# Kernel tuning notes

Hardware: AMD Instinct MI355X
Metric: run time of the kernel (lower is better)

The kernel has to match this reference:

```python
import jax, jax.numpy as jnp
import numpy as np

H_SIZE = 2048
NUM_K_HEADS = 16
NUM_V_HEADS = 32
DK = 128
DV = 128
KEY_DIM = NUM_K_HEADS * DK        # 2048
VALUE_DIM = NUM_V_HEADS * DV      # 4096
CONV_DIM = 2 * KEY_DIM + VALUE_DIM  # 8192
KERNEL = 4
EPS = 1e-6
B, S = 2, 2048


def setup_inputs() -> dict:
    key = jax.random.key(0)
    ks = jax.random.split(key, 8)
    w = lambda k, shape, s: jax.random.normal(k, shape, jnp.float32) * s
    return {
        "hidden_states": jax.random.normal(ks[0], (B, S, H_SIZE), jnp.float32),
        "w_qkv": w(ks[1], (H_SIZE, CONV_DIM), 0.02),
        "w_z": w(ks[2], (H_SIZE, VALUE_DIM), 0.02),
        "w_b": w(ks[3], (H_SIZE, NUM_V_HEADS), 0.02),
        "w_a": w(ks[4], (H_SIZE, NUM_V_HEADS), 0.02),
        "conv_w": w(ks[5], (CONV_DIM, KERNEL), 0.2),
        "dt_bias": jnp.ones((NUM_V_HEADS,), jnp.float32),
        "A_log": jnp.zeros((NUM_V_HEADS,), jnp.float32),
        "norm_gamma": jnp.ones((DV,), jnp.float32),
        "w_out": w(ks[6], (VALUE_DIM, H_SIZE), 0.02),
    }


def _l2norm(x, eps=1e-6):
    return x * jax.lax.rsqrt(jnp.sum(x * x, axis=-1, keepdims=True) + eps)


def _causal_conv(x, w):
    # depthwise causal conv1d; x: (B,S,C), w: (C,K)
    K = w.shape[-1]
    Sq = x.shape[1]
    xp = jnp.pad(x, ((0, 0), (K - 1, 0), (0, 0)))
    out = xp[:, 0:Sq, :] * w[None, None, :, 0]
    for j in range(1, K):  # tiny fixed kernel loop (K=4)
        out = out + xp[:, j:j + Sq, :] * w[None, None, :, j]
    return out


def _forward(hidden_states, w_qkv, w_z, w_b, w_a, conv_w, dt_bias, A_log,
             norm_gamma, w_out):
    Bq, Sq, _ = hidden_states.shape
    mixed = hidden_states @ w_qkv                       # (B,S,CONV_DIM)
    z = (hidden_states @ w_z).reshape(Bq, Sq, NUM_V_HEADS, DV)
    b = hidden_states @ w_b                             # (B,S,Hv)
    a = hidden_states @ w_a                             # (B,S,Hv)
    mixed = jax.nn.silu(_causal_conv(mixed, conv_w))
    q, k, v = jnp.split(mixed, [KEY_DIM, 2 * KEY_DIM], axis=-1)
    q = q.reshape(Bq, Sq, NUM_K_HEADS, DK)
    k = k.reshape(Bq, Sq, NUM_K_HEADS, DK)
    v = v.reshape(Bq, Sq, NUM_V_HEADS, DV)
    nrep = NUM_V_HEADS // NUM_K_HEADS
    q = jnp.repeat(q, nrep, axis=2)                     # GQA expand -> Hv heads
    k = jnp.repeat(k, nrep, axis=2)
    beta = jax.nn.sigmoid(b)                            # write gate
    g = -jnp.exp(A_log)[None, None, :] * jax.nn.softplus(a + dt_bias[None, None, :])

    # gated delta rule recurrence in float32 (matches reference)
    qf = _l2norm(q.astype(jnp.float32)) * (DK ** -0.5)
    kf = _l2norm(k.astype(jnp.float32))
    vf = v.astype(jnp.float32)
    gf = g.astype(jnp.float32)
    bf = beta.astype(jnp.float32)

    def step(state, xs):
        q_t, k_t, v_t, g_t, b_t = xs  # (B,H,dk),(B,H,dk),(B,H,dv),(B,H),(B,H)
        state = state * jnp.exp(g_t)[..., None, None]
        kv = jnp.einsum('bhk,bhkv->bhv', k_t, state)
        delta = (v_t - kv) * b_t[..., None]
        state = state + jnp.einsum('bhk,bhv->bhkv', k_t, delta)
        out = jnp.einsum('bhk,bhkv->bhv', q_t, state)
        return state, out

    mv = lambda x: jnp.moveaxis(x, 1, 0)  # (B,S,...) -> (S,B,...)
    xs = (mv(qf), mv(kf), mv(vf), mv(gf), mv(bf))
    state0 = jnp.zeros((Bq, NUM_V_HEADS, DK, DV), jnp.float32)
    _, outs = jax.lax.scan(step, state0, xs)            # (S,B,H,dv)
    o = jnp.moveaxis(outs, 0, 1)                        # (B,S,H,dv)

    # gated RMSNorm over head_v_dim: gate with silu(z), then rms-normalize
    o = o * jax.nn.silu(z.astype(jnp.float32))
    o = o * jax.lax.rsqrt(jnp.mean(o * o, axis=-1, keepdims=True) + EPS)
    o = o * norm_gamma
    o = o.reshape(Bq, Sq, VALUE_DIM).astype(hidden_states.dtype)
    return o @ w_out


def reference(hidden_states, w_qkv, w_z, w_b, w_a, conv_w, dt_bias, A_log,
              norm_gamma, w_out):
    return _forward(hidden_states, w_qkv, w_z, w_b, w_a, conv_w, dt_bias,
                    A_log, norm_gamma, w_out)
```

## Files before the change

kernel.cpp:

```cpp
#include <hip/hip_runtime.h>
#include <hip/hip_bf16.h>
#include <cstdint>


#define HSZ 2048
#define NUM_K_HEADS 16
#define NUM_V_HEADS 32
#define DKH 128
#define DVH 128
#define KEY_DIM 2048
#define VALUE_DIM 4096
#define CONV_DIM 8192
#define BB 2
#define SSEQ 2048
#define MM (BB * SSEQ)
#define CHUNK 64
#define NCHUNK (SSEQ / CHUNK)
#define DVB 16

typedef __hip_bfloat16 bf16;
typedef short short8 __attribute__((ext_vector_type(8)));
typedef float f32x4 __attribute__((ext_vector_type(4)));

__device__ __forceinline__ float bfu(ushort u) {
  union { float f; uint32_t i; } x;
  x.i = ((uint32_t)u) << 16;
  return x.f;
}
__device__ __forceinline__ ushort f2b(float f) {
  bf16 h = __float2bfloat16(f);
  return *reinterpret_cast<ushort*>(&h);
}

__device__ __forceinline__ void gload16(const void* g, const void* l) {
  __builtin_amdgcn_global_load_lds(
      (const __attribute__((address_space(1))) unsigned int*)g,
      (__attribute__((address_space(3))) unsigned int*)(const_cast<void*>(l)),
      16, 0, 0);
}

__device__ __forceinline__ int kidx(int r, int d) {
  return r * 128 + (((d >> 3) ^ (r & 7)) << 3) + (d & 7);
}
__device__ __forceinline__ int widx(int r, int d) {
  return r * 64 + (((d >> 3) ^ (r & 7)) << 3) + (d & 7);
}

__global__ __launch_bounds__(256) void cast_bf16_kernel(
    const float* __restrict__ in, ushort* __restrict__ out, int n4) {
  int i = blockIdx.x * 256 + threadIdx.x;
  if (i < n4) {
    float4 v = ((const float4*)in)[i];
    ushort4 u;
    u.x = f2b(v.x); u.y = f2b(v.y); u.z = f2b(v.z); u.w = f2b(v.w);
    ((ushort4*)out)[i] = u;
  }
}

__global__ __launch_bounds__(256) void transpose_cast(
    const float* __restrict__ W, ushort* __restrict__ WT, int K, int N) {
  __shared__ ushort tile[32][33];
  const int tx = threadIdx.x & 31, ty = threadIdx.x >> 5;
  const int n0 = blockIdx.x * 32, k0 = blockIdx.y * 32;
#pragma unroll
  for (int i = 0; i < 4; ++i)
    tile[ty + i * 8][tx] = f2b(W[(size_t)(k0 + ty + i * 8) * N + n0 + tx]);
  __syncthreads();
#pragma unroll
  for (int i = 0; i < 4; ++i)
    WT[(size_t)(n0 + ty + i * 8) * K + k0 + tx] = tile[tx][ty + i * 8];
}

__global__ __launch_bounds__(512) void gemm256_fused(
    const ushort* __restrict__ A, const ushort* __restrict__ BT,
    ushort* __restrict__ Cm, ushort* __restrict__ Cz, int M, int K) {
  __shared__ __align__(16) ushort smem[256 * 264];
  const int t = threadIdx.x;
  const int w = t >> 6, lane = t & 63;
  const int m0 = blockIdx.y * 256, n0 = blockIdx.x * 256;
  const int wm = (w >> 2) * 128, wn = (w & 3) * 64;
  const int fr = lane & 15, kb = lane >> 4;
  const int srow = t >> 2;
  const int sg = t & 3;
  const int ssw = ((sg ^ ((srow >> 1) & 3)) << 3);
  f32x4 acc[8][4] = {};
  const int nt = K / 32;

#define STAGE_F(tt, buf)                                                      \
  {                                                                           \
    const int k0_ = (tt)*32;                                                  \
    ushort* As_ = smem + (buf)*16384;                                         \
    ushort* Bs_ = As_ + 8192;                                                 \
    _Pragma("unroll") for (int p = 0; p < 2; ++p) {                           \
      const int row_ = p * 128 + srow;                                        \
      gload16(&A[(size_t)(m0 + row_) * K + k0_ + ssw],                        \
              &As_[row_ * 32 + sg * 8]);                                      \
    }                                                                         \
    _Pragma("unroll") for (int p = 0; p < 2; ++p) {                           \
      const int row_ = p * 128 + srow;                                        \
      gload16(&BT[(size_t)(n0 + row_) * K + k0_ + ssw],                       \
              &Bs_[row_ * 32 + sg * 8]);                                      \
    }                                                                         \
  }

  STAGE_F(0, 0);
  STAGE_F(1, 1);

  for (int tt = 0; tt < nt; ++tt) {
    const int buf = tt & 3;
    if (tt + 1 < nt)
      asm volatile("s_waitcnt vmcnt(4)" ::: "memory");
    else
      asm volatile("s_waitcnt vmcnt(0)" ::: "memory");
    __builtin_amdgcn_sched_barrier(0);
    __builtin_amdgcn_s_barrier();
    __builtin_amdgcn_sched_barrier(0);
    if (tt + 2 < nt) STAGE_F(tt + 2, (tt + 2) & 3);
    const ushort* As = smem + buf * 16384;
    const ushort* Bs = As + 8192;
    short8 af[8], bf_[4];
#pragma unroll
    for (int nf = 0; nf < 4; ++nf) {
      const int row = wn + nf * 16 + fr;
      bf_[nf] = *(const short8*)&Bs[row * 32 + ((kb ^ ((row >> 1) & 3)) << 3)];
    }
#pragma unroll
    for (int mf = 0; mf < 8; ++mf) {
      const int row = wm + mf * 16 + fr;
      af[mf] = *(const short8*)&As[row * 32 + ((kb ^ ((row >> 1) & 3)) << 3)];
    }
#pragma unroll
    for (int mf = 0; mf < 8; ++mf)
#pragma unroll
      for (int nf = 0; nf < 4; ++nf)
        acc[mf][nf] = __builtin_amdgcn_mfma_f32_16x16x32_bf16(
            af[mf], bf_[nf], acc[mf][nf], 0, 0, 0);
  }
#undef STAGE_F

  __syncthreads();
  const int crow = wm + (lane >> 4) * 4;
  const int ccol = wn + fr;
#pragma unroll
  for (int mf = 0; mf < 8; ++mf)
#pragma unroll
    for (int nf = 0; nf < 4; ++nf)
#pragma unroll
      for (int j = 0; j < 4; ++j)
        smem[(crow + mf * 16 + j) * 264 + ccol + nf * 16] = f2b(acc[mf][nf][j]);
  __syncthreads();
  ushort* Cout = (n0 < CONV_DIM) ? Cm : Cz;
  const int Nout = (n0 < CONV_DIM) ? CONV_DIM : VALUE_DIM;
  const int ncol = (n0 < CONV_DIM) ? n0 : n0 - CONV_DIM;
#pragma unroll
  for (int p = 0; p < 16; ++p) {
    const int r = p * 16 + (t >> 5), cch = (t & 31) * 8;
    *(short8*)&Cout[(size_t)(m0 + r) * Nout + ncol + cch] =
        *(const short8*)&smem[r * 264 + cch];
  }
}

__global__ __launch_bounds__(256, 2) void gemm128_f32(
    const ushort* __restrict__ A, const ushort* __restrict__ BT,
    float* __restrict__ C, int M, int N, int K) {
  __shared__ __align__(16) ushort smem[4 * 8192];
  const int t = threadIdx.x;
  const int w = t >> 6, lane = t & 63;
  const int m0 = blockIdx.y * 128, n0 = blockIdx.x * 128;
  const int wm = (w >> 1) * 64, wn = (w & 1) * 64;
  const int fr = lane & 15, kb = lane >> 4;
  const int srow = t >> 2;
  const int sg = t & 3;
  const int ssw = ((sg ^ ((srow >> 1) & 3)) << 3);
  f32x4 acc[4][4] = {};
  const int nt = K / 32;

#define STAGE_G(tt, buf)                                                      \
  {                                                                           \
    const int k0_ = (tt)*32;                                                  \
    ushort* As_ = smem + (buf)*8192;                                          \
    ushort* Bs_ = As_ + 4096;                                                 \
    _Pragma("unroll") for (int p = 0; p < 2; ++p) {                           \
      const int row_ = p * 64 + srow;                                         \
      gload16(&A[(size_t)(m0 + row_) * K + k0_ + ssw],                        \
              &As_[row_ * 32 + sg * 8]);                                      \
    }                                                                         \
    _Pragma("unroll") for (int p = 0; p < 2; ++p) {                           \
      const int row_ = p * 64 + srow;                                         \
      gload16(&BT[(size_t)(n0 + row_) * K + k0_ + ssw],                       \
              &Bs_[row_ * 32 + sg * 8]);                                      \
    }                                                                         \
  }

  STAGE_G(0, 0);
  STAGE_G(1, 1);

  for (int tt = 0; tt < nt; ++tt) {
    const int buf = tt & 3;
    if (tt + 1 < nt)
      asm volatile("s_waitcnt vmcnt(4)" ::: "memory");
    else
      asm volatile("s_waitcnt vmcnt(0)" ::: "memory");
    __builtin_amdgcn_sched_barrier(0);
    __builtin_amdgcn_s_barrier();
    __builtin_amdgcn_sched_barrier(0);
    if (tt + 2 < nt) STAGE_G(tt + 2, (tt + 2) & 3);
    const ushort* As = smem + buf * 8192;
    const ushort* Bs = As + 4096;
    short8 af[4], bfr[4];
#pragma unroll
    for (int nf = 0; nf < 4; ++nf) {
      const int row = wn + nf * 16 + fr;
      bfr[nf] = *(const short8*)&Bs[row * 32 + ((kb ^ ((row >> 1) & 3)) << 3)];
    }
#pragma unroll
    for (int mf = 0; mf < 4; ++mf) {
      const int row = wm + mf * 16 + fr;
      af[mf] = *(const short8*)&As[row * 32 + ((kb ^ ((row >> 1) & 3)) << 3)];
    }
#pragma unroll
    for (int mf = 0; mf < 4; ++mf)
#pragma unroll
      for (int nf = 0; nf < 4; ++nf)
        acc[mf][nf] = __builtin_amdgcn_mfma_f32_16x16x32_bf16(
            af[mf], bfr[nf], acc[mf][nf], 0, 0, 0);
  }
#undef STAGE_G

  const int orow = m0 + wm + (lane >> 4) * 4;
  const int ocol = n0 + wn + fr;
#pragma unroll
  for (int mf = 0; mf < 4; ++mf)
#pragma unroll
    for (int nf = 0; nf < 4; ++nf)
#pragma unroll
      for (int j = 0; j < 4; ++j)
        C[(size_t)(orow + mf * 16 + j) * N + ocol + nf * 16] = acc[mf][nf][j];
}

__global__ __launch_bounds__(256) void ba_kernel(
    const float* __restrict__ hs, const float* __restrict__ w_b,
    const float* __restrict__ w_a, const float* __restrict__ dt_bias,
    const float* __restrict__ A_log, float* __restrict__ gbuf,
    float* __restrict__ beta) {
  const int row0 = blockIdx.x * 8;
  const int t = threadIdx.x;
  __shared__ float hsr[8][HSZ];
  __shared__ float red[2][256];
  {
    const float4* src = (const float4*)(hs + (size_t)row0 * HSZ);
    for (int i = t; i < 8 * HSZ / 4; i += 256) ((float4*)hsr)[i] = src[i];
  }
  __syncthreads();
  const int h = t & 31, p = t >> 5;
  float sb[8] = {}, sa[8] = {};
  const int kbeg = p * 256;
  for (int k = kbeg; k < kbeg + 256; ++k) {
    float wb = w_b[k * NUM_V_HEADS + h];
    float wa = w_a[k * NUM_V_HEADS + h];
#pragma unroll
    for (int r = 0; r < 8; ++r) {
      float x = hsr[r][k];
      sb[r] += x * wb;
      sa[r] += x * wa;
    }
  }
#pragma unroll
  for (int r = 0; r < 8; ++r) {
    red[0][t] = sb[r];
    red[1][t] = sa[r];
    __syncthreads();
    if (t < NUM_V_HEADS) {
      float b = 0.f, a = 0.f;
#pragma unroll
      for (int q = 0; q < 8; ++q) {
        b += red[0][t + 32 * q];
        a += red[1][t + 32 * q];
      }
      float bet = 1.f / (1.f + expf(-b));
      float x = a + dt_bias[t];
      float sp = (x > 20.f) ? x : log1pf(expf(x));
      gbuf[(size_t)(row0 + r) * NUM_V_HEADS + t] = -expf(A_log[t]) * sp;
      beta[(size_t)(row0 + r) * NUM_V_HEADS + t] = bet;
    }
    __syncthreads();
  }
}

__global__ __launch_bounds__(256) void conv_kernel(
    const ushort* __restrict__ mixed, const float* __restrict__ conv_w,
    ushort* __restrict__ qkv) {
  const int bid = blockIdx.x;
  const int slice = bid & 3;
  const int row0 = (bid >> 2) * 8;
  const int s0 = row0 & (SSEQ - 1);
  const int t = threadIdx.x;
  const int cbase = slice * 2048 + t * 8;

  float wreg[4][8];
#pragma unroll
  for (int e = 0; e < 8; ++e) {
    float4 wv = *(const float4*)&conv_w[(cbase + e) * 4];
    wreg[0][e] = wv.x;
    wreg[1][e] = wv.y;
    wreg[2][e] = wv.z;
    wreg[3][e] = wv.w;
  }

  const ushort* mp = mixed + (size_t)row0 * CONV_DIM + cbase;
  short8 win[4];
  const short8 z8 = {0, 0, 0, 0, 0, 0, 0, 0};
#pragma unroll
  for (int j = 0; j < 3; ++j)
    win[j] = (s0 - 3 + j >= 0) ? *(const short8*)&mp[(ptrdiff_t)(j - 3) * CONV_DIM]
                               : z8;

  if (slice < 2) {
    float vals[8][8];
    float ssq[8];
#pragma unroll
    for (int r = 0; r < 8; ++r) {
      win[3] = *(const short8*)&mp[(ptrdiff_t)r * CONV_DIM];
      float sq = 0.f;
#pragma unroll
      for (int e = 0; e < 8; ++e) {
        float a = bfu((ushort)win[0][e]) * wreg[0][e] +
                  bfu((ushort)win[1][e]) * wreg[1][e] +
                  bfu((ushort)win[2][e]) * wreg[2][e] +
                  bfu((ushort)win[3][e]) * wreg[3][e];
        float x = a / (1.f + expf(-a));
        vals[r][e] = x;
        sq += x * x;
      }
      ssq[r] = sq;
      win[0] = win[1];
      win[1] = win[2];
      win[2] = win[3];
    }
#pragma unroll
    for (int r = 0; r < 8; ++r) {
      float sq = ssq[r];
      sq += __shfl_xor(sq, 1, 64);
      sq += __shfl_xor(sq, 2, 64);
      sq += __shfl_xor(sq, 4, 64);
      sq += __shfl_xor(sq, 8, 64);
      float sc = rsqrtf(sq + 1e-6f);
      if (slice == 0) sc *= 0.08838834764831845f;
      short8 o;
#pragma unroll
      for (int e = 0; e < 8; ++e) o[e] = (short)f2b(vals[r][e] * sc);
      *(short8*)&qkv[(size_t)(row0 + r) * CONV_DIM + cbase] = o;
    }
  } else {
#pragma unroll
    for (int r = 0; r < 8; ++r) {
      win[3] = *(const short8*)&mp[(ptrdiff_t)r * CONV_DIM];
      short8 o;
#pragma unroll
      for (int e = 0; e < 8; ++e) {
        float a = bfu((ushort)win[0][e]) * wreg[0][e] +
                  bfu((ushort)win[1][e]) * wreg[1][e] +
                  bfu((ushort)win[2][e]) * wreg[2][e] +
                  bfu((ushort)win[3][e]) * wreg[3][e];
        o[e] = (short)f2b(a / (1.f + expf(-a)));
      }
      *(short8*)&qkv[(size_t)(row0 + r) * CONV_DIM + cbase] = o;
      win[0] = win[1];
      win[1] = win[2];
      win[2] = win[3];
    }
  }
}

__global__ __launch_bounds__(256) void chunk_T_kernel(
    const ushort* __restrict__ qkv, const float* __restrict__ gbuf,
    const float* __restrict__ beta, ushort* __restrict__ Tbuf,
    ushort* __restrict__ Wbuf) {
  const int bid = blockIdx.x;
  const int c = bid & 31;
  const int h = (bid >> 5) & 31;
  const int b = bid >> 10;
  const int hk = h >> 1;
  const int t = threadIdx.x;
  const int w = t >> 6, lane = t & 63;
  const int fr = lane & 15, fq = lane >> 4;

  __shared__ ushort Klds[64 * 128];
  __shared__ ushort Qlds[64 * 128];
  __shared__ __align__(16) float AT[64][68];
  __shared__ ushort Wlds[64 * 64];
  __shared__ float Gs[64], Bsh[64];

  const int row0 = b * SSEQ + c * CHUNK;
  const int qcol = hk * DKH;
  const int kcol = KEY_DIM + hk * DKH;

#pragma unroll
  for (int r = 0; r < 4; ++r) {
    int vi = t + 256 * r;
    int row = vi >> 4, gr = vi & 15;
    const size_t gb = (size_t)(row0 + row) * CONV_DIM;
    *(short8*)&Klds[row * 128 + ((gr ^ (row & 7)) << 3)] =
        *(const short8*)&qkv[gb + kcol + gr * 8];
    *(short8*)&Qlds[row * 128 + ((gr ^ (row & 7)) << 3)] =
        *(const short8*)&qkv[gb + qcol + gr * 8];
  }
  if (t < 64) {
    float s = gbuf[(size_t)(row0 + t) * NUM_V_HEADS + h];
#pragma unroll
    for (int off = 1; off < 64; off <<= 1) {
      float p = __shfl_up(s, off, 64);
      if (lane >= off) s += p;
    }
    Gs[t] = s;
    Bsh[t] = beta[(size_t)(row0 + t) * NUM_V_HEADS + h];
  }
  __syncthreads();

  f32x4 kkt[4] = {}, qkt[4] = {};
#pragma unroll
  for (int ks = 0; ks < 4; ++ks) {
    int d0 = ks * 32 + fq * 8;
    short8 xk = *(const short8*)&Klds[kidx(w * 16 + fr, d0)];
    short8 xq = *(const short8*)&Qlds[kidx(w * 16 + fr, d0)];
#pragma unroll
    for (int j = 0; j < 4; ++j) {
      short8 yk = *(const short8*)&Klds[kidx(j * 16 + fr, d0)];
      kkt[j] = __builtin_amdgcn_mfma_f32_16x16x32_bf16(xk, yk, kkt[j], 0, 0, 0);
      qkt[j] = __builtin_amdgcn_mfma_f32_16x16x32_bf16(xq, yk, qkt[j], 0, 0, 0);
    }
  }
#pragma unroll
  for (int j = 0; j < 4; ++j)
#pragma unroll
    for (int jj = 0; jj < 4; ++jj) {
      int i = w * 16 + fq * 4 + jj;
      int jc = j * 16 + fr;
      AT[jc][i] = (jc < i) ? Bsh[i] * __expf(Gs[i] - Gs[jc]) * kkt[j][jj] : 0.f;
      float val = (jc <= i) ? __expf(Gs[i] - Gs[jc]) * qkt[j][jj] : 0.f;
      Wlds[widx(i, jc)] = f2b(val);
    }
  __syncthreads();

  {
    ushort* Wg = Wbuf + (size_t)bid * 4096;
#pragma unroll
    for (int e = 0; e < 8; ++e)
      ((uint*)Wg)[e * 256 + t] = ((const uint*)Wlds)[e * 256 + t];
  }

  if (w == 0) {
    float u[64];
#pragma unroll
    for (int i = 0; i < 64; ++i) u[i] = (i == lane) ? 1.f : 0.f;
#pragma unroll
    for (int j = 0; j < 63; ++j) {
      float xj = u[j];
      const int i0 = (j + 1) & ~3;
#pragma unroll
      for (int ii = i0; ii < 64; ii += 4) {
        float4 a4 = *(const float4*)&AT[j][ii];
        if (ii + 0 > j) u[ii + 0] -= a4.x * xj;
        if (ii + 1 > j) u[ii + 1] -= a4.y * xj;
        if (ii + 2 > j) u[ii + 2] -= a4.z * xj;
        if (ii + 3 > j) u[ii + 3] -= a4.w * xj;
      }
    }
    ushort* Tg = Tbuf + (size_t)bid * 4096;
#pragma unroll
    for (int i = 0; i < 64; ++i) Tg[i * 64 + lane] = f2b(u[i]);
  }
}

__global__ __launch_bounds__(256, 2) void recur_chunk_kernel(
    const ushort* __restrict__ qkv, const float* __restrict__ gbuf,
    const float* __restrict__ beta, const ushort* __restrict__ Tbuf,
    const ushort* __restrict__ Wbuf, float* __restrict__ o) {
  const int bid = blockIdx.x;
  const int dvq = bid & 7;
  const int h = (bid >> 3) & 31;
  const int b = bid >> 8;
  const int hk = h >> 1;
  const int t = threadIdx.x;
  const int w = t >> 6, lane = t & 63;
  const int fr = lane & 15, fq = lane >> 4;

  __shared__ ushort Klds[64 * 128];
  __shared__ ushort Vlds[64 * DVB];
  __shared__ ushort Sth[DVB * 128];
  __shared__ ushort Stl[DVB * 128];
  __shared__ ushort Th[64 * 64];
  __shared__ ushort Wlds[64 * 64];
  __shared__ ushort Ut[DVB * 64];
  __shared__ ushort UTs[DVB * 64];
  __shared__ ushort UTo[DVB * 64];
  __shared__ float Gs[64], Bsh[64];

  float sreg[2][4] = {};

  const int qcol = hk * DKH;
  const int kcol = KEY_DIM + hk * DKH;
  const int vcol = 2 * KEY_DIM + h * DVH + dvq * DVB;
  const int ocol = h * DVH + dvq * DVB;
  const size_t tbase0 = ((size_t)(b * 32 + h) * 32) * 4096;

  short8 pK[4], pT0, pT1, pV, pxq[4];
  uint pW[8];
  float pg = 0.f, pb = 0.f;

  auto prefetch = [&](int c) {
    const int row0 = b * SSEQ + c * CHUNK;
#pragma unroll
    for (int ks = 0; ks < 4; ++ks)
      pxq[ks] = *(const short8*)&qkv[(size_t)(row0 + w * 16 + fr) * CONV_DIM +
                                     qcol + ks * 32 + fq * 8];
    const ushort* Tg = Tbuf + tbase0 + (size_t)c * 4096;
    const ushort* Wg = Wbuf + tbase0 + (size_t)c * 4096;
    pT0 = *(const short8*)&Tg[t * 16];
    pT1 = *(const short8*)&Tg[t * 16 + 8];
#pragma unroll
    for (int e = 0; e < 8; ++e) pW[e] = ((const uint*)Wg)[e * 256 + t];
#pragma unroll
    for (int r = 0; r < 4; ++r) {
      int vi = t + 256 * r;
      int row = vi >> 4, gr = vi & 15;
      pK[r] = *(const short8*)&qkv[(size_t)(row0 + row) * CONV_DIM + kcol + gr * 8];
    }
    if (t < 128) {
      int row = t >> 1, c0 = (t & 1) * 8;
      pV = *(const short8*)&qkv[(size_t)(row0 + row) * CONV_DIM + vcol + c0];
    }
    if (t < 64) {
      pg = gbuf[(size_t)(row0 + t) * NUM_V_HEADS + h];
      pb = beta[(size_t)(row0 + t) * NUM_V_HEADS + h];
    }
  };

  prefetch(0);

  for (int c = 0; c < NCHUNK; ++c) {
    const int row0 = b * SSEQ + c * CHUNK;

    short8 xq[4];
#pragma unroll
    for (int ks = 0; ks < 4; ++ks) xq[ks] = pxq[ks];
#pragma unroll
    for (int e = 0; e < 8; ++e) ((uint*)Wlds)[e * 256 + t] = pW[e];
#pragma unroll
    for (int r = 0; r < 4; ++r) {
      int vi = t + 256 * r;
      int row = vi >> 4, gr = vi & 15;
      *(short8*)&Klds[row * 128 + ((gr ^ (row & 7)) << 3)] = pK[r];
    }
    if (t < 128) {
      int row = t >> 1, c0 = (t & 1) * 8;
      *(short8*)&Vlds[row * DVB + c0] = pV;
    }
    if (t < 64) {
      float s = pg;
#pragma unroll
      for (int off = 1; off < 64; off <<= 1) {
        float p = __shfl_up(s, off, 64);
        if (lane >= off) s += p;
      }
      Gs[t] = s;
      Bsh[t] = pb;
    }
#pragma unroll
    for (int dt = 0; dt < 2; ++dt)
#pragma unroll
      for (int jj = 0; jj < 4; ++jj) {
        int d = (w * 2 + dt) * 16 + fq * 4 + jj;
        float f = sreg[dt][jj];
        ushort hi = f2b(f);
        int idx = kidx(fr, d);
        Sth[idx] = hi;
        Stl[idx] = f2b(f - bfu(hi));
      }
    {
      int r = t >> 2, d0 = (t & 3) * 16;
      *(short8*)&Th[widx(r, d0)] = pT0;
      *(short8*)&Th[widx(r, d0 + 8)] = pT1;
    }
    __syncthreads();

    if (c + 1 < NCHUNK) prefetch(c + 1);

    f32x4 ks0 = {}, qs0 = {};
#pragma unroll
    for (int ks = 0; ks < 4; ++ks) {
      int d0 = ks * 32 + fq * 8;
      short8 xk = *(const short8*)&Klds[kidx(w * 16 + fr, d0)];
      short8 yh = *(const short8*)&Sth[kidx(fr, d0)];
      short8 yl = *(const short8*)&Stl[kidx(fr, d0)];
      ks0 = __builtin_amdgcn_mfma_f32_16x16x32_bf16(xk, yh, ks0, 0, 0, 0);
      ks0 = __builtin_amdgcn_mfma_f32_16x16x32_bf16(xk, yl, ks0, 0, 0, 0);
      qs0 = __builtin_amdgcn_mfma_f32_16x16x32_bf16(xq[ks], yh, qs0, 0, 0, 0);
      qs0 = __builtin_amdgcn_mfma_f32_16x16x32_bf16(xq[ks], yl, qs0, 0, 0, 0);
    }
    f32x4 oacc;
#pragma unroll
    for (int jj = 0; jj < 4; ++jj) {
      int i = w * 16 + fq * 4 + jj;
      float eg = __expf(Gs[i]);
      float rhs = Bsh[i] * (bfu(Vlds[i * DVB + fr]) - eg * ks0[jj]);
      Ut[widx(fr, i)] = f2b(rhs);
      oacc[jj] = qs0[jj] * eg;
    }
    __syncthreads();

    {
      f32x4 uacc = {};
#pragma unroll
      for (int ks = 0; ks < 2; ++ks) {
        int j0 = ks * 32 + fq * 8;
        short8 ta = *(const short8*)&Th[widx(w * 16 + fr, j0)];
        short8 ub = *(const short8*)&Ut[widx(fr, j0)];
        uacc = __builtin_amdgcn_mfma_f32_16x16x32_bf16(ta, ub, uacc, 0, 0, 0);
      }
#pragma unroll
      for (int jj = 0; jj < 4; ++jj) {
        int i = w * 16 + fq * 4 + jj;
        float u = uacc[jj];
        UTo[widx(fr, i)] = f2b(u);
        UTs[widx(fr, i)] = f2b(u * __expf(Gs[63] - Gs[i]));
      }
    }
    __syncthreads();

#pragma unroll
    for (int ks = 0; ks < 2; ++ks) {
      int i0 = ks * 32 + fq * 8;
      short8 xw = *(const short8*)&Wlds[widx(w * 16 + fr, i0)];
      short8 yu = *(const short8*)&UTo[widx(fr, i0)];
      oacc = __builtin_amdgcn_mfma_f32_16x16x32_bf16(xw, yu, oacc, 0, 0, 0);
    }
#pragma unroll
    for (int jj = 0; jj < 4; ++jj) {
      int tt = w * 16 + fq * 4 + jj;
      o[(size_t)(row0 + tt) * VALUE_DIM + ocol + fr] = oacc[jj];
    }
    {
      float eGC = __expf(Gs[63]);
#pragma unroll
      for (int dt = 0; dt < 2; ++dt) {
        const int dk0 = (w * 2 + dt) * 16;
        f32x4 sacc;
#pragma unroll
        for (int jj = 0; jj < 4; ++jj) sacc[jj] = sreg[dt][jj] * eGC;
        const int dkr = dk0 + fr;
#pragma unroll
        for (int ks = 0; ks < 2; ++ks) {
          short8 xk;
#pragma unroll
          for (int e = 0; e < 8; ++e)
            xk[e] = (short)Klds[kidx(ks * 32 + fq * 8 + e, dkr)];
          short8 yu = *(const short8*)&UTs[widx(fr, ks * 32 + fq * 8)];
          sacc = __builtin_amdgcn_mfma_f32_16x16x32_bf16(xk, yu, sacc, 0, 0, 0);
        }
#pragma unroll
        for (int jj = 0; jj < 4; ++jj) sreg[dt][jj] = sacc[jj];
      }
    }
    __syncthreads();
  }
}

__global__ __launch_bounds__(256) void gnorm_kernel(
    const float* __restrict__ o, const ushort* __restrict__ z,
    const float* __restrict__ gamma, ushort* __restrict__ ob) {
  const int row = blockIdx.x;
  const int t = threadIdx.x;
  const int grp = t >> 3, r = t & 7;
  const float* op = o + (size_t)row * VALUE_DIM + grp * DVH + r * 16;
  const ushort* zp = z + (size_t)row * VALUE_DIM + grp * DVH + r * 16;
  ushort* obp = ob + (size_t)row * VALUE_DIM + grp * DVH + r * 16;
  float4 ov[4];
  short8 zv[2];
#pragma unroll
  for (int q = 0; q < 4; ++q) ov[q] = *(const float4*)&op[q * 4];
  zv[0] = *(const short8*)&zp[0];
  zv[1] = *(const short8*)&zp[8];
  float vals[16];
  float ssq = 0.f;
#pragma unroll
  for (int i = 0; i < 16; ++i) {
    float zz = bfu((ushort)zv[i >> 3][i & 7]);
    float oo = ((const float*)&ov[i >> 2])[i & 3];
    float x = oo * (zz / (1.f + expf(-zz)));
    vals[i] = x;
    ssq += x * x;
  }
  ssq += __shfl_xor(ssq, 1, 64);
  ssq += __shfl_xor(ssq, 2, 64);
  ssq += __shfl_xor(ssq, 4, 64);
  float sc = rsqrtf(ssq * (1.f / 128.f) + 1e-6f);
  short8 o0, o1;
#pragma unroll
  for (int i = 0; i < 8; ++i) {
    o0[i] = (short)f2b(vals[i] * sc * gamma[r * 16 + i]);
    o1[i] = (short)f2b(vals[8 + i] * sc * gamma[r * 16 + 8 + i]);
  }
  *(short8*)&obp[0] = o0;
  *(short8*)&obp[8] = o1;
}

extern "C" void kernel_launch(void* const* d_in, const int* in_sizes, int n_in,
                              void* d_out, int out_size, void* d_ws,
                              size_t ws_size, hipStream_t stream) {
  const float* hs = (const float*)d_in[0];
  const float* w_qkv = (const float*)d_in[1];
  const float* w_z = (const float*)d_in[2];
  const float* w_b = (const float*)d_in[3];
  const float* w_a = (const float*)d_in[4];
  const float* conv_w = (const float*)d_in[5];
  const float* dt_bias = (const float*)d_in[6];
  const float* A_log = (const float*)d_in[7];
  const float* gamma = (const float*)d_in[8];
  const float* w_out = (const float*)d_in[9];
  float* out = (float*)d_out;
  char* wsb = (char*)d_ws;

  ushort* hs_b = (ushort*)wsb;
  ushort* wqkvT = hs_b + (size_t)MM * HSZ;
  ushort* wzT = wqkvT + (size_t)CONV_DIM * HSZ;
  ushort* woutT = wzT + (size_t)VALUE_DIM * HSZ;
  ushort* mixed = woutT + (size_t)HSZ * VALUE_DIM;
  ushort* qkv = mixed + (size_t)MM * CONV_DIM;
  ushort* z = qkv + (size_t)MM * CONV_DIM;
  float* gbuf = (float*)(z + (size_t)MM * VALUE_DIM);
  float* beta = gbuf + (size_t)MM * NUM_V_HEADS;
  float* o = (float*)mixed;
  ushort* ob = qkv;
  ushort* Tbuf = hs_b;
  ushort* Wbuf = wqkvT;

  cast_bf16_kernel<<<(MM * HSZ / 4 + 255) / 256, 256, 0, stream>>>(
      hs, hs_b, MM * HSZ / 4);
  transpose_cast<<<dim3(CONV_DIM / 32, HSZ / 32), 256, 0, stream>>>(
      w_qkv, wqkvT, HSZ, CONV_DIM);
  transpose_cast<<<dim3(VALUE_DIM / 32, HSZ / 32), 256, 0, stream>>>(
      w_z, wzT, HSZ, VALUE_DIM);
  transpose_cast<<<dim3(HSZ / 32, VALUE_DIM / 32), 256, 0, stream>>>(
      w_out, woutT, VALUE_DIM, HSZ);

  gemm256_fused<<<dim3((CONV_DIM + VALUE_DIM) / 256, MM / 256), 512, 0,
                  stream>>>(hs_b, wqkvT, mixed, z, MM, HSZ);
  ba_kernel<<<MM / 8, 256, 0, stream>>>(hs, w_b, w_a, dt_bias, A_log, gbuf,
                                        beta);
  conv_kernel<<<2048, 256, 0, stream>>>(mixed, conv_w, qkv);
  chunk_T_kernel<<<2048, 256, 0, stream>>>(qkv, gbuf, beta, Tbuf, Wbuf);
  recur_chunk_kernel<<<512, 256, 0, stream>>>(qkv, gbuf, beta, Tbuf, Wbuf, o);
  gnorm_kernel<<<MM, 256, 0, stream>>>(o, z, gamma, ob);
  gemm128_f32<<<dim3(HSZ / 128, MM / 128), 256, 0, stream>>>(
      ob, woutT, out, MM, HSZ, VALUE_DIM);
}
```

Baseline: 699.4 us.

## Merge prep casts into one kernel, raise MFMA priority, drop Q LDS staging

The hidden-state cast and the three weight transpose-casts are merged into a single prep kernel launch, which removes three launch gaps. Both GEMM main loops wrap their MFMA block in s_setprio(1)/s_setprio(0) so waves in the math phase get issue priority over waves doing loads. chunk_T_kernel now loads its Q fragments straight from global memory into registers instead of staging them through LDS, which cuts shared memory use and may allow higher occupancy. The cost is less coalesced Q loads and more register pressure.

```diff
diff --git a/kernel.cpp b/kernel.cpp
--- a/kernel.cpp
+++ b/kernel.cpp
@@ -46,22 +46,11 @@
   return r * 64 + (((d >> 3) ^ (r & 7)) << 3) + (d & 7);
 }
 
-__global__ __launch_bounds__(256) void cast_bf16_kernel(
-    const float* __restrict__ in, ushort* __restrict__ out, int n4) {
-  int i = blockIdx.x * 256 + threadIdx.x;
-  if (i < n4) {
-    float4 v = ((const float4*)in)[i];
-    ushort4 u;
-    u.x = f2b(v.x); u.y = f2b(v.y); u.z = f2b(v.z); u.w = f2b(v.w);
-    ((ushort4*)out)[i] = u;
-  }
-}
-
-__global__ __launch_bounds__(256) void transpose_cast(
-    const float* __restrict__ W, ushort* __restrict__ WT, int K, int N) {
-  __shared__ ushort tile[32][33];
-  const int tx = threadIdx.x & 31, ty = threadIdx.x >> 5;
-  const int n0 = blockIdx.x * 32, k0 = blockIdx.y * 32;
+__device__ __forceinline__ void tc_tile(const float* __restrict__ W,
+                                        ushort* __restrict__ WT, int K, int N,
+                                        int n0, int k0, int t,
+                                        ushort (*tile)[33]) {
+  const int tx = t & 31, ty = t >> 5;
 #pragma unroll
   for (int i = 0; i < 4; ++i)
     tile[ty + i * 8][tx] = f2b(W[(size_t)(k0 + ty + i * 8) * N + n0 + tx]);
@@ -69,6 +58,35 @@
 #pragma unroll
   for (int i = 0; i < 4; ++i)
     WT[(size_t)(n0 + ty + i * 8) * K + k0 + tx] = tile[tx][ty + i * 8];
+}
+
+__global__ __launch_bounds__(256) void prep_kernel(
+    const float* __restrict__ hs, const float* __restrict__ w_qkv,
+    const float* __restrict__ w_z, const float* __restrict__ w_out,
+    ushort* __restrict__ hs_b, ushort* __restrict__ wqkvT,
+    ushort* __restrict__ wzT, ushort* __restrict__ woutT) {
+  __shared__ ushort tile[32][33];
+  const int bid = blockIdx.x;
+  const int t = threadIdx.x;
+  if (bid < 8192) {
+    const int i = bid * 256 + t;
+    float4 v = ((const float4*)hs)[i];
+    ushort4 u;
+    u.x = f2b(v.x); u.y = f2b(v.y); u.z = f2b(v.z); u.w = f2b(v.w);
+    ((ushort4*)hs_b)[i] = u;
+  } else if (bid < 8192 + 16384) {
+    const int idx = bid - 8192;
+    tc_tile(w_qkv, wqkvT, HSZ, CONV_DIM, (idx & 255) * 32, (idx >> 8) * 32, t,
+            tile);
+  } else if (bid < 8192 + 16384 + 8192) {
+    const int idx = bid - 24576;
+    tc_tile(w_z, wzT, HSZ, VALUE_DIM, (idx & 127) * 32, (idx >> 7) * 32, t,
+            tile);
+  } else {
+    const int idx = bid - 32768;
+    tc_tile(w_out, woutT, VALUE_DIM, HSZ, (idx & 63) * 32, (idx >> 6) * 32, t,
+            tile);
+  }
 }
 
 __global__ __launch_bounds__(512) void gemm256_fused(
@@ -129,12 +147,14 @@
       const int row = wm + mf * 16 + fr;
       af[mf] = *(const short8*)&As[row * 32 + ((kb ^ ((row >> 1) & 3)) << 3)];
     }
+    __builtin_amdgcn_s_setprio(1);
 #pragma unroll
     for (int mf = 0; mf < 8; ++mf)
 #pragma unroll
       for (int nf = 0; nf < 4; ++nf)
         acc[mf][nf] = __builtin_amdgcn_mfma_f32_16x16x32_bf16(
             af[mf], bf_[nf], acc[mf][nf], 0, 0, 0);
+    __builtin_amdgcn_s_setprio(0);
   }
 #undef STAGE_F
 
@@ -218,12 +238,14 @@
       const int row = wm + mf * 16 + fr;
       af[mf] = *(const short8*)&As[row * 32 + ((kb ^ ((row >> 1) & 3)) << 3)];
     }
+    __builtin_amdgcn_s_setprio(1);
 #pragma unroll
     for (int mf = 0; mf < 4; ++mf)
 #pragma unroll
       for (int nf = 0; nf < 4; ++nf)
         acc[mf][nf] = __builtin_amdgcn_mfma_f32_16x16x32_bf16(
             af[mf], bfr[nf], acc[mf][nf], 0, 0, 0);
+    __builtin_amdgcn_s_setprio(0);
   }
 #undef STAGE_G
 
@@ -386,7 +408,6 @@
   const int fr = lane & 15, fq = lane >> 4;
 
   __shared__ ushort Klds[64 * 128];
-  __shared__ ushort Qlds[64 * 128];
   __shared__ __align__(16) float AT[64][68];
   __shared__ ushort Wlds[64 * 64];
   __shared__ float Gs[64], Bsh[64];
@@ -395,15 +416,17 @@
   const int qcol = hk * DKH;
   const int kcol = KEY_DIM + hk * DKH;
 
+  short8 xq[4];
+#pragma unroll
+  for (int ks = 0; ks < 4; ++ks)
+    xq[ks] = *(const short8*)&qkv[(size_t)(row0 + w * 16 + fr) * CONV_DIM +
+                                  qcol + ks * 32 + fq * 8];
 #pragma unroll
   for (int r = 0; r < 4; ++r) {
     int vi = t + 256 * r;
     int row = vi >> 4, gr = vi & 15;
-    const size_t gb = (size_t)(row0 + row) * CONV_DIM;
     *(short8*)&Klds[row * 128 + ((gr ^ (row & 7)) << 3)] =
-        *(const short8*)&qkv[gb + kcol + gr * 8];
-    *(short8*)&Qlds[row * 128 + ((gr ^ (row & 7)) << 3)] =
-        *(const short8*)&qkv[gb + qcol + gr * 8];
+        *(const short8*)&qkv[(size_t)(row0 + row) * CONV_DIM + kcol + gr * 8];
   }
   if (t < 64) {
     float s = gbuf[(size_t)(row0 + t) * NUM_V_HEADS + h];
@@ -422,12 +445,11 @@
   for (int ks = 0; ks < 4; ++ks) {
     int d0 = ks * 32 + fq * 8;
     short8 xk = *(const short8*)&Klds[kidx(w * 16 + fr, d0)];
-    short8 xq = *(const short8*)&Qlds[kidx(w * 16 + fr, d0)];
 #pragma unroll
     for (int j = 0; j < 4; ++j) {
       short8 yk = *(const short8*)&Klds[kidx(j * 16 + fr, d0)];
       kkt[j] = __builtin_amdgcn_mfma_f32_16x16x32_bf16(xk, yk, kkt[j], 0, 0, 0);
-      qkt[j] = __builtin_amdgcn_mfma_f32_16x16x32_bf16(xq, yk, qkt[j], 0, 0, 0);
+      qkt[j] = __builtin_amdgcn_mfma_f32_16x16x32_bf16(xq[ks], yk, qkt[j], 0, 0, 0);
     }
   }
 #pragma unroll
@@ -735,14 +757,8 @@
   ushort* Tbuf = hs_b;
   ushort* Wbuf = wqkvT;
 
-  cast_bf16_kernel<<<(MM * HSZ / 4 + 255) / 256, 256, 0, stream>>>(
-      hs, hs_b, MM * HSZ / 4);
-  transpose_cast<<<dim3(CONV_DIM / 32, HSZ / 32), 256, 0, stream>>>(
-      w_qkv, wqkvT, HSZ, CONV_DIM);
-  transpose_cast<<<dim3(VALUE_DIM / 32, HSZ / 32), 256, 0, stream>>>(
-      w_z, wzT, HSZ, VALUE_DIM);
-  transpose_cast<<<dim3(HSZ / 32, VALUE_DIM / 32), 256, 0, stream>>>(
-      w_out, woutT, VALUE_DIM, HSZ);
+  prep_kernel<<<40960, 256, 0, stream>>>(hs, w_qkv, w_z, w_out, hs_b, wqkvT,
+                                         wzT, woutT);
 
   gemm256_fused<<<dim3((CONV_DIM + VALUE_DIM) / 256, MM / 256), 512, 0,
                   stream>>>(hs_b, wqkvT, mixed, z, MM, HSZ);
```

Result: faster. 674.2 us (-3.6%).
